# Kernel optimization log

Measured on AMD Instinct MI355X. Metric: run time of the kernel, lower is better.

The kernel has to match this reference:

```python
import jax, jax.numpy as jnp
import numpy as np

B, S, D, H = 4, 1024, 1024, 16  # batch, seq_len, num_hiddens, num_heads
NEG = -1e6  # mask value used by the source's _sequence_mask


def setup_inputs() -> dict:
    key = jax.random.key(0)
    ks = jax.random.split(key, 8)
    f = lambda k, sh: (jax.random.normal(k, sh, dtype=jnp.float32) * 0.02)
    return {
        "queries": f(ks[0], (B, S, D)),
        "keys": f(ks[1], (B, S, D)),
        "values": f(ks[2], (B, S, D)),
        "valid_lens": jax.random.randint(ks[3], (B,), 1, S + 1),
        "Wq": f(ks[4], (D, D)),
        "Wk": f(ks[5], (D, D)),
        "Wv": f(ks[6], (D, D)),
        "Wo": f(ks[7], (D, D)),
    }


def reference(queries, keys, values, valid_lens, Wq, Wk, Wv, Wo):
    dh = D // H

    def split_heads(x):  # [B,S,D] -> [B,H,S,dh]
        return x.reshape(B, S, H, dh).transpose(0, 2, 1, 3)

    q = split_heads(queries @ Wq)
    k = split_heads(keys @ Wk)
    v = split_heads(values @ Wv)

    scores = jnp.einsum("bhqd,bhkd->bhqk", q, k) / jnp.sqrt(jnp.float32(dh))
    # per-batch key mask broadcast over heads and query positions: [B,1,1,S]
    mask = (jnp.arange(S)[None, :] < valid_lens[:, None])[:, None, None, :]
    scores = jnp.where(mask, scores, NEG)        # pre-softmax set to -1e6
    attn = jax.nn.softmax(scores, axis=-1)
    attn = jnp.where(mask, attn, 0.0)            # post-softmax zeroing (source quirk)
    out = jnp.einsum("bhqk,bhkd->bhqd", attn, v)  # [B,H,S,dh]
    # source uses permute(0,2,3,1): head-interleaved concat order
    concat = out.transpose(0, 2, 3, 1).reshape(B, S, D)
    return concat @ Wo
```

## Files before the change

### kernel.cpp

```cpp
#include <hip/hip_runtime.h>
#include <hip/hip_bf16.h>

#define BB 4
#define SS 1024
#define DDIM 1024
#define HH 16
#define MROWS (BB * SS)

typedef __attribute__((ext_vector_type(8))) short bf16x8;
typedef __attribute__((ext_vector_type(4))) float f32x4;

static __device__ __forceinline__ short f2bf(float x) {
    union { __hip_bfloat16 h; short s; } u;
    u.h = __float2bfloat16(x);
    return u.s;
}

#define GL_LDS16(gp, lp)                                                      \
    __builtin_amdgcn_global_load_lds(                                         \
        (const __attribute__((address_space(1))) void*)(gp),                  \
        (__attribute__((address_space(3))) void*)(lp), 16, 0, 0)

#define SWZ8(row, s) (((s) ^ ((row) & 7)) << 3)

static __device__ __forceinline__ void transposeW_body(const float* __restrict__ W,
                                                       short* __restrict__ dst,
                                                       int k0, int n0,
                                                       short (*sT)[72], int t) {
    {
        int r = t >> 2, cq = (t & 3) << 4;
        const float* p = W + (size_t)(k0 + r) * DDIM + n0 + cq;
        float4 a = ((const float4*)p)[0], b = ((const float4*)p)[1];
        float4 c = ((const float4*)p)[2], d = ((const float4*)p)[3];
        short* dp = &sT[r][cq];
        dp[0]  = f2bf(a.x); dp[1]  = f2bf(a.y); dp[2]  = f2bf(a.z); dp[3]  = f2bf(a.w);
        dp[4]  = f2bf(b.x); dp[5]  = f2bf(b.y); dp[6]  = f2bf(b.z); dp[7]  = f2bf(b.w);
        dp[8]  = f2bf(c.x); dp[9]  = f2bf(c.y); dp[10] = f2bf(c.z); dp[11] = f2bf(c.w);
        dp[12] = f2bf(d.x); dp[13] = f2bf(d.y); dp[14] = f2bf(d.z); dp[15] = f2bf(d.w);
    }
    __syncthreads();
    {
        int n = t >> 2, kq = (t & 3) << 4;
        bf16x8 o0, o1;
#pragma unroll
        for (int j = 0; j < 8; ++j) o0[j] = sT[kq + j][n];
#pragma unroll
        for (int j = 0; j < 8; ++j) o1[j] = sT[kq + 8 + j][n];
        short* q = dst + (size_t)(n0 + n) * DDIM + k0 + kq;
        *(bf16x8*)q = o0;
        *(bf16x8*)(q + 8) = o1;
    }
}

__global__ __launch_bounds__(256) void prep(const float* __restrict__ X0,
                                            const float* __restrict__ X1,
                                            const float* __restrict__ X2,
                                            const float* __restrict__ W0,
                                            const float* __restrict__ W1,
                                            const float* __restrict__ W2,
                                            short* __restrict__ dstA,
                                            short* __restrict__ Wt,
                                            const int* __restrict__ vlens) {
    __shared__ short sT[64][72];
    const int bx = blockIdx.x;
    const int t = threadIdx.x;
    if (bx >= 6144) {
        const int w = bx - 6144;
        const int z = w >> 8;
        const int rem = w & 255;
        const float* W = (z == 0) ? W0 : (z == 1) ? W1 : W2;
        transposeW_body(W, Wt + (size_t)z * DDIM * DDIM,
                        (rem >> 4) * 64, (rem & 15) * 64, sT, t);
        return;
    }
    const int z = bx >> 11;
    const int blk = bx & 2047;
    const int row0 = blk << 1;
    if (z >= 1) {
        const int bb = row0 >> 10;
        if ((row0 & 1023) >= vlens[bb]) return;
    }
    const float* X = (z == 0) ? X0 : (z == 1) ? X1 : X2;
    short* D = dstA + (size_t)z * MROWS * DDIM;
    const size_t base = (size_t)blk * 2048 + t * 8;
    const float4 x0 = ((const float4*)(X + base))[0];
    const float4 x1 = ((const float4*)(X + base))[1];
    bf16x8 vv;
    vv[0] = f2bf(x0.x); vv[1] = f2bf(x0.y); vv[2] = f2bf(x0.z); vv[3] = f2bf(x0.w);
    vv[4] = f2bf(x1.x); vv[5] = f2bf(x1.y); vv[6] = f2bf(x1.z); vv[7] = f2bf(x1.w);
    *(bf16x8*)(D + base) = vv;
}

__global__ __launch_bounds__(256) void post(const short* __restrict__ v,
                                            short* __restrict__ vT,
                                            const float* __restrict__ Wo,
                                            short* __restrict__ wt_o,
                                            const int* __restrict__ vlens) {
    __shared__ short sT[64][72];
    const int t = threadIdx.x;
    const int z = blockIdx.z;
    if (z == 4) {
        transposeW_body(Wo, wt_o, blockIdx.y * 64, blockIdx.x * 64, sT, t);
        return;
    }
    const int st = blockIdx.x, h = blockIdx.y, bb = z;
    if (st * 64 >= vlens[bb]) return;
#pragma unroll
    for (int j = 0; j < 2; ++j) {
        int c = t + j * 256;
        int sr = c >> 3, co = (c & 7) << 3;
        *(bf16x8*)(&sT[sr][co]) =
            *(const bf16x8*)(v + (size_t)(bb * SS + st * 64 + sr) * DDIM + h * 64 + co);
    }
    __syncthreads();
    {
        int e = t >> 2, sq = (t & 3) << 4;
        bf16x8 o0, o1;
#pragma unroll
        for (int j = 0; j < 8; ++j) o0[j] = sT[sq + j][e];
#pragma unroll
        for (int j = 0; j < 8; ++j) o1[j] = sT[sq + 8 + j][e];
        short* dst = vT + ((size_t)(bb * HH + h) * 64 + e) * SS + st * 64 + sq;
        *(bf16x8*)dst = o0;
        *(bf16x8*)(dst + 8) = o1;
    }
}

__global__ __launch_bounds__(256) void transposeW3(const float* __restrict__ W0,
                                                   const float* __restrict__ W1,
                                                   const float* __restrict__ W2,
                                                   short* __restrict__ Wt) {
    __shared__ short sT[64][72];
    const int z = blockIdx.z;
    const float* W = (z == 0) ? W0 : (z == 1) ? W1 : W2;
    transposeW_body(W, Wt + (size_t)z * DDIM * DDIM,
                    blockIdx.y * 64, blockIdx.x * 64, sT, threadIdx.x);
}

__global__ __launch_bounds__(256) void transposeV(const short* __restrict__ v,
                                                  short* __restrict__ vT,
                                                  const int* __restrict__ vlens) {
    const int st = blockIdx.x, h = blockIdx.y, bb = blockIdx.z;
    if (st * 64 >= vlens[bb]) return;
    __shared__ short sT[64][72];
    const int t = threadIdx.x;
#pragma unroll
    for (int j = 0; j < 2; ++j) {
        int c = t + j * 256;
        int sr = c >> 3, co = (c & 7) << 3;
        *(bf16x8*)(&sT[sr][co]) =
            *(const bf16x8*)(v + (size_t)(bb * SS + st * 64 + sr) * DDIM + h * 64 + co);
    }
    __syncthreads();
    {
        int e = t >> 2, sq = (t & 3) << 4;
        bf16x8 o0, o1;
#pragma unroll
        for (int j = 0; j < 8; ++j) o0[j] = sT[sq + j][e];
#pragma unroll
        for (int j = 0; j < 8; ++j) o1[j] = sT[sq + 8 + j][e];
        short* dst = vT + ((size_t)(bb * HH + h) * 64 + e) * SS + st * 64 + sq;
        *(bf16x8*)dst = o0;
        *(bf16x8*)(dst + 8) = o1;
    }
}

template<bool A_F32, bool C_F32, int BN, bool SKIP>
__global__ __launch_bounds__(256) void gemm(const void* __restrict__ A0v,
                                            const void* __restrict__ A1v,
                                            const void* __restrict__ A2v,
                                            const short* __restrict__ BtBase,
                                            void* __restrict__ C0v,
                                            void* __restrict__ C1v,
                                            void* __restrict__ C2v,
                                            const int* __restrict__ vlens) {
    constexpr int NJ  = BN / 32;
    constexpr int NBX = DDIM / BN;
    constexpr int NPB = 32 * NBX;
    constexpr int BCH = BN / 32;

    __shared__ short sA[128 * 64];
    __shared__ short sB[BN * 64];

    const int tid = threadIdx.x;
    const int lane = tid & 63, wid = tid >> 6;
    const int wr = wid >> 1, wc = wid & 1;
    const int g = lane >> 4, l15 = lane & 15;

    const int blk = blockIdx.x;
    const int z = blk / NPB;
    const int inner = blk % NPB;
    const int xcd = inner & 7, ii = inner >> 3;
    const int by = xcd * 4 + ii / NBX;
    const int bx = ii % NBX;

    if constexpr (SKIP) {
        if (z >= 1 && ((by & 7) << 7) >= vlens[by >> 3]) return;
    }

    const void* Av = (z == 0) ? A0v : (z == 1) ? A1v : A2v;
    const short* Bt = BtBase + (size_t)z * DDIM * DDIM;
    void* Cv = (z == 0) ? C0v : (z == 1) ? C1v : C2v;
    const float* Af = (const float*)Av;
    const short* Ab = (const short*)Av;
    const int K = DDIM;

    f32x4 acc[4][NJ] = {};
    const int nkt = K >> 6;

    for (int t = 0; t < nkt; ++t) {
        const int kt = t << 6;
        __syncthreads();

        if constexpr (A_F32) {
            float4 ra[4][2];
#pragma unroll
            for (int j = 0; j < 4; ++j) {
                int c = tid + j * 256;
                int row = c >> 3, s = c & 7;
                const float* p = Af + (size_t)(by * 128 + row) * K + kt + s * 8;
                ra[j][0] = ((const float4*)p)[0];
                ra[j][1] = ((const float4*)p)[1];
            }
#pragma unroll
            for (int j = 0; j < 4; ++j) {
                int c = tid + j * 256;
                int row = c >> 3, s = c & 7;
                bf16x8 vv;
                vv[0] = f2bf(ra[j][0].x); vv[1] = f2bf(ra[j][0].y);
                vv[2] = f2bf(ra[j][0].z); vv[3] = f2bf(ra[j][0].w);
                vv[4] = f2bf(ra[j][1].x); vv[5] = f2bf(ra[j][1].y);
                vv[6] = f2bf(ra[j][1].z); vv[7] = f2bf(ra[j][1].w);
                *(bf16x8*)(&sA[row * 64 + SWZ8(row, s)]) = vv;
            }
        } else {
#pragma unroll
            for (int j = 0; j < 4; ++j) {
                int c = tid + j * 256;
                int row = c >> 3, sp = c & 7;
                GL_LDS16(Ab + (size_t)(by * 128 + row) * K + kt + SWZ8(row, sp),
                         (char*)&sA[0] + c * 16);
            }
        }
#pragma unroll
        for (int j = 0; j < BCH; ++j) {
            int c = tid + j * 256;
            int row = c >> 3, sp = c & 7;
            GL_LDS16(Bt + (size_t)(bx * BN + row) * K + kt + SWZ8(row, sp),
                     (char*)&sB[0] + c * 16);
        }
        __syncthreads();

        bf16x8 af[4][2], bfr[NJ][2];
#pragma unroll
        for (int i = 0; i < 4; ++i) {
            int row = wr * 64 + i * 16 + l15;
#pragma unroll
            for (int kh = 0; kh < 2; ++kh) {
                int s = kh * 4 + g;
                af[i][kh] = *(const bf16x8*)(&sA[row * 64 + SWZ8(row, s)]);
            }
        }
#pragma unroll
        for (int j = 0; j < NJ; ++j) {
            int row = wc * (BN / 2) + j * 16 + l15;
#pragma unroll
            for (int kh = 0; kh < 2; ++kh) {
                int s = kh * 4 + g;
                bfr[j][kh] = *(const bf16x8*)(&sB[row * 64 + SWZ8(row, s)]);
            }
        }
#pragma unroll
        for (int kh = 0; kh < 2; ++kh)
#pragma unroll
            for (int i = 0; i < 4; ++i)
#pragma unroll
                for (int j = 0; j < NJ; ++j)
                    acc[i][j] = __builtin_amdgcn_mfma_f32_16x16x32_bf16(af[i][kh], bfr[j][kh], acc[i][j], 0, 0, 0);
    }

#pragma unroll
    for (int i = 0; i < 4; ++i)
#pragma unroll
        for (int j = 0; j < NJ; ++j)
#pragma unroll
            for (int r = 0; r < 4; ++r) {
                int row = by * 128 + wr * 64 + i * 16 + g * 4 + r;
                int col = bx * BN + wc * (BN / 2) + j * 16 + l15;
                if constexpr (C_F32)
                    ((float*)Cv)[(size_t)row * DDIM + col] = acc[i][j][r];
                else
                    ((short*)Cv)[(size_t)row * DDIM + col] = f2bf(acc[i][j][r]);
            }
}

template<bool TRV>
__global__ __launch_bounds__(256) void attn(const short* __restrict__ q,
                                            const short* __restrict__ k,
                                            const short* __restrict__ v,
                                            const int* __restrict__ vlens,
                                            short* __restrict__ att) {
    const int blk = blockIdx.x;
    const int qt = blk >> 6;
    const int hb = blk & 63;
    const int bb = hb & 3;
    const int h  = hb >> 2;

    const int tid = threadIdx.x;
    const int lane = tid & 63, wid = tid >> 6;
    const int g = lane >> 4, l15 = lane & 15;
    const int vlen = vlens[bb];

    __shared__ short sK[2][64 * 64];
    __shared__ short sV[2][64 * 64];
    __shared__ short sP[4][16 * 64];

    const int srow = qt * 64 + wid * 16 + l15;
    const short* qrow = q + ((size_t)(bb * SS + srow)) * DDIM + h * 64;
    bf16x8 qf[2];
    qf[0] = *(const bf16x8*)(qrow + g * 8);
    qf[1] = *(const bf16x8*)(qrow + 32 + g * 8);

    float lsum[4] = {0.f, 0.f, 0.f, 0.f};
    f32x4 oacc[4] = {};

    const int key0 = tid >> 3, key1 = (tid + 256) >> 3, sp = tid & 7;
    const int d0 = (tid & 7) << 3;
    const short* vTb = v + ((size_t)(bb * HH + h) * 64) * SS;

    const int ntiles = (vlen + 63) >> 6;

    {
        GL_LDS16(k + ((size_t)(bb * SS + key0)) * DDIM + h * 64 + ((sp ^ (key0 & 7)) << 3),
                 (char*)&sK[0][0] + tid * 16);
        GL_LDS16(k + ((size_t)(bb * SS + key1)) * DDIM + h * 64 + ((sp ^ (key1 & 7)) << 3),
                 (char*)&sK[0][0] + (tid + 256) * 16);
        if constexpr (TRV) {
            GL_LDS16(vTb + (size_t)key0 * SS + ((sp ^ (key0 & 7)) << 3),
                     (char*)&sV[0][0] + tid * 16);
            GL_LDS16(vTb + (size_t)key1 * SS + ((sp ^ (key1 & 7)) << 3),
                     (char*)&sV[0][0] + (tid + 256) * 16);
        } else {
            bf16x8 v0 = *(const bf16x8*)(v + ((size_t)(bb * SS + key0)) * DDIM + h * 64 + d0);
            bf16x8 v1 = *(const bf16x8*)(v + ((size_t)(bb * SS + key1)) * DDIM + h * 64 + d0);
#pragma unroll
            for (int e = 0; e < 8; ++e) {
                int e0 = d0 + e;
                sV[0][e0 * 64 + (((key0 >> 3) ^ (e0 & 7)) << 3) + (key0 & 7)] = v0[e];
                sV[0][e0 * 64 + (((key1 >> 3) ^ (e0 & 7)) << 3) + (key1 & 7)] = v1[e];
            }
        }
    }
    __syncthreads();

    for (int t = 0; t < ntiles; ++t) {
        const int cur = t & 1, nxt = cur ^ 1;
        const int kb = t * 64;
        const bool pre = (t + 1 < ntiles);

        bf16x8 vr0, vr1;
        if (pre) {
            const int kb2 = kb + 64;
            GL_LDS16(k + ((size_t)(bb * SS + kb2 + key0)) * DDIM + h * 64 + ((sp ^ (key0 & 7)) << 3),
                     (char*)&sK[nxt][0] + tid * 16);
            GL_LDS16(k + ((size_t)(bb * SS + kb2 + key1)) * DDIM + h * 64 + ((sp ^ (key1 & 7)) << 3),
                     (char*)&sK[nxt][0] + (tid + 256) * 16);
            if constexpr (TRV) {
                GL_LDS16(vTb + (size_t)key0 * SS + kb2 + ((sp ^ (key0 & 7)) << 3),
                         (char*)&sV[nxt][0] + tid * 16);
                GL_LDS16(vTb + (size_t)key1 * SS + kb2 + ((sp ^ (key1 & 7)) << 3),
                         (char*)&sV[nxt][0] + (tid + 256) * 16);
            } else {
                vr0 = *(const bf16x8*)(v + ((size_t)(bb * SS + kb2 + key0)) * DDIM + h * 64 + d0);
                vr1 = *(const bf16x8*)(v + ((size_t)(bb * SS + kb2 + key1)) * DDIM + h * 64 + d0);
            }
        }

        f32x4 sacc[4] = {};
#pragma unroll
        for (int kg = 0; kg < 4; ++kg) {
            int row = kg * 16 + l15;
#pragma unroll
            for (int kh = 0; kh < 2; ++kh) {
                int s = kh * 4 + g;
                bf16x8 kf = *(const bf16x8*)(&sK[cur][row * 64 + ((s ^ (row & 7)) << 3)]);
                sacc[kg] = __builtin_amdgcn_mfma_f32_16x16x32_bf16(qf[kh], kf, sacc[kg], 0, 0, 0);
            }
        }

#pragma unroll
        for (int r = 0; r < 4; ++r) {
            float p[4], ls = 0.f;
#pragma unroll
            for (int kg = 0; kg < 4; ++kg) {
                float s = fminf(sacc[kg][r] * 0.125f, 60.0f);
                if (kb + kg * 16 + l15 >= vlen) s = -1e30f;
                p[kg] = __expf(s);
                ls += p[kg];
            }
            lsum[r] += ls;
            const int srw = g * 4 + r;
#pragma unroll
            for (int kg = 0; kg < 4; ++kg) {
                int col = kg * 16 + l15;
                sP[wid][srw * 64 + (((col >> 3) ^ (srw & 7)) << 3) + (col & 7)] = f2bf(p[kg]);
            }
        }

        bf16x8 pf[2];
#pragma unroll
        for (int kh = 0; kh < 2; ++kh) {
            int s = kh * 4 + g;
            pf[kh] = *(const bf16x8*)(&sP[wid][l15 * 64 + ((s ^ (l15 & 7)) << 3)]);
        }
#pragma unroll
        for (int n = 0; n < 4; ++n) {
            const int e = n * 16 + l15;
#pragma unroll
            for (int kh = 0; kh < 2; ++kh) {
                int s = kh * 4 + g;
                bf16x8 vf = *(const bf16x8*)(&sV[cur][e * 64 + ((s ^ (e & 7)) << 3)]);
                oacc[n] = __builtin_amdgcn_mfma_f32_16x16x32_bf16(pf[kh], vf, oacc[n], 0, 0, 0);
            }
        }

        if constexpr (!TRV) {
            if (pre) {
#pragma unroll
                for (int e = 0; e < 8; ++e) {
                    int e0 = d0 + e;
                    sV[nxt][e0 * 64 + (((key0 >> 3) ^ (e0 & 7)) << 3) + (key0 & 7)] = vr0[e];
                    sV[nxt][e0 * 64 + (((key1 >> 3) ^ (e0 & 7)) << 3) + (key1 & 7)] = vr1[e];
                }
            }
        }
        __syncthreads();
    }

#pragma unroll
    for (int r = 0; r < 4; ++r) {
        float rs = lsum[r];
#pragma unroll
        for (int off = 1; off < 16; off <<= 1)
            rs += __shfl_xor(rs, off);
        lsum[r] = rs;
    }

#pragma unroll
    for (int n = 0; n < 4; ++n)
#pragma unroll
        for (int r = 0; r < 4; ++r) {
            float o = oacc[n][r] / lsum[r];
            int sg = qt * 64 + wid * 16 + g * 4 + r;
            int e = n * 16 + l15;
            att[((size_t)(bb * SS + sg)) * DDIM + e * HH + h] = f2bf(o);
        }
}

extern "C" void kernel_launch(void* const* d_in, const int* in_sizes, int n_in,
                              void* d_out, int out_size, void* d_ws, size_t ws_size,
                              hipStream_t stream) {
    const float* queries = (const float*)d_in[0];
    const float* keys    = (const float*)d_in[1];
    const float* values  = (const float*)d_in[2];
    const int*   vlens   = (const int*)d_in[3];
    const float* Wq      = (const float*)d_in[4];
    const float* Wk      = (const float*)d_in[5];
    const float* Wv      = (const float*)d_in[6];
    const float* Wo      = (const float*)d_in[7];
    float* out = (float*)d_out;

    short* ws = (short*)d_ws;
    const size_t sz = (size_t)MROWS * DDIM;
    short* q_ws   = ws;
    short* k_ws   = ws + sz;
    short* v_ws   = ws + 2 * sz;
    short* att_ws = ws + 3 * sz;
    short* wt3  = att_ws;

    const size_t regionB = sz * sizeof(short);
    const bool big = ws_size >= 7 * regionB;
    const bool mid = ws_size >= 5 * regionB;

    if (big) {
        short* qb = ws + 4 * sz;
        short* kb = ws + 5 * sz;
        short* vb = ws + 6 * sz;
        prep<<<dim3(6912), 256, 0, stream>>>(queries, keys, values,
                                             Wq, Wk, Wv, qb, wt3, vlens);
        gemm<false, false, 128, true><<<dim3(768), 256, 0, stream>>>(
            qb, kb, vb, wt3, q_ws, k_ws, v_ws, vlens);
        post<<<dim3(16, 16, 5), 256, 0, stream>>>(v_ws, qb, Wo, vb, vlens);
        attn<true><<<dim3(1024), 256, 0, stream>>>(q_ws, k_ws, qb, vlens, att_ws);
        gemm<false, true, 64, false><<<dim3(512), 256, 0, stream>>>(
            att_ws, att_ws, att_ws, vb, out, out, out, vlens);
    } else if (mid) {
        short* vT = ws + 4 * sz;
        short* wt_o = q_ws;
        transposeW3<<<dim3(16, 16, 3), 256, 0, stream>>>(Wq, Wk, Wv, wt3);
        gemm<true, false, 128, true><<<dim3(768), 256, 0, stream>>>(
            queries, keys, values, wt3, q_ws, k_ws, v_ws, vlens);
        transposeV<<<dim3(16, 16, 4), 256, 0, stream>>>(v_ws, vT, vlens);
        attn<true><<<dim3(1024), 256, 0, stream>>>(q_ws, k_ws, vT, vlens, att_ws);
        transposeW3<<<dim3(16, 16, 1), 256, 0, stream>>>(Wo, Wo, Wo, wt_o);
        gemm<false, true, 64, false><<<dim3(512), 256, 0, stream>>>(
            att_ws, att_ws, att_ws, wt_o, out, out, out, vlens);
    } else {
        short* wt_o = q_ws;
        transposeW3<<<dim3(16, 16, 3), 256, 0, stream>>>(Wq, Wk, Wv, wt3);
        gemm<true, false, 128, true><<<dim3(768), 256, 0, stream>>>(
            queries, keys, values, wt3, q_ws, k_ws, v_ws, vlens);
        attn<false><<<dim3(1024), 256, 0, stream>>>(q_ws, k_ws, v_ws, vlens, att_ws);
        transposeW3<<<dim3(16, 16, 1), 256, 0, stream>>>(Wo, Wo, Wo, wt_o);
        gemm<false, true, 64, false><<<dim3(512), 256, 0, stream>>>(
            att_ws, att_ws, att_ws, wt_o, out, out, out, vlens);
    }
}
```

Before: 94.66 us.

## Fuse V transpose into QKV GEMM epilogue and Wo transpose into attention

The QKV projection GEMM now writes V directly in head-transposed layout by staging its tile through shared memory in the epilogue, and the Wo weight transpose runs as extra blocks prepended to the attention launch. Together these remove the separate post kernel and its launch, plus a full round-trip of V through global memory. In exchange the GEMM epilogue for V gains an extra LDS pass and barrier, and the attention kernel uses one merged shared buffer and a larger grid.

```diff
diff --git a/kernel.cpp b/kernel.cpp
--- a/kernel.cpp
+++ b/kernel.cpp
@@ -91,41 +91,6 @@
     *(bf16x8*)(D + base) = vv;
 }
 
-__global__ __launch_bounds__(256) void post(const short* __restrict__ v,
-                                            short* __restrict__ vT,
-                                            const float* __restrict__ Wo,
-                                            short* __restrict__ wt_o,
-                                            const int* __restrict__ vlens) {
-    __shared__ short sT[64][72];
-    const int t = threadIdx.x;
-    const int z = blockIdx.z;
-    if (z == 4) {
-        transposeW_body(Wo, wt_o, blockIdx.y * 64, blockIdx.x * 64, sT, t);
-        return;
-    }
-    const int st = blockIdx.x, h = blockIdx.y, bb = z;
-    if (st * 64 >= vlens[bb]) return;
-#pragma unroll
-    for (int j = 0; j < 2; ++j) {
-        int c = t + j * 256;
-        int sr = c >> 3, co = (c & 7) << 3;
-        *(bf16x8*)(&sT[sr][co]) =
-            *(const bf16x8*)(v + (size_t)(bb * SS + st * 64 + sr) * DDIM + h * 64 + co);
-    }
-    __syncthreads();
-    {
-        int e = t >> 2, sq = (t & 3) << 4;
-        bf16x8 o0, o1;
-#pragma unroll
-        for (int j = 0; j < 8; ++j) o0[j] = sT[sq + j][e];
-#pragma unroll
-        for (int j = 0; j < 8; ++j) o1[j] = sT[sq + 8 + j][e];
-        short* dst = vT + ((size_t)(bb * HH + h) * 64 + e) * SS + st * 64 + sq;
-        *(bf16x8*)dst = o0;
-        *(bf16x8*)(dst + 8) = o1;
-    }
-}
-
 __global__ __launch_bounds__(256) void transposeW3(const float* __restrict__ W0,
                                                    const float* __restrict__ W1,
                                                    const float* __restrict__ W2,
@@ -165,7 +130,7 @@
     }
 }
 
-template<bool A_F32, bool C_F32, int BN, bool SKIP>
+template<bool A_F32, bool C_F32, int BN, bool SKIP, bool TRC>
 __global__ __launch_bounds__(256) void gemm(const void* __restrict__ A0v,
                                             const void* __restrict__ A1v,
                                             const void* __restrict__ A2v,
@@ -179,8 +144,9 @@
     constexpr int NPB = 32 * NBX;
     constexpr int BCH = BN / 32;
 
-    __shared__ short sA[128 * 64];
-    __shared__ short sB[BN * 64];
+    __shared__ short smem[128 * 64 + BN * 64];
+    short* sA = smem;
+    short* sB = smem + 128 * 64;
 
     const int tid = threadIdx.x;
     const int lane = tid & 63, wid = tid >> 6;
@@ -239,7 +205,7 @@
                 int c = tid + j * 256;
                 int row = c >> 3, sp = c & 7;
                 GL_LDS16(Ab + (size_t)(by * 128 + row) * K + kt + SWZ8(row, sp),
-                         (char*)&sA[0] + c * 16);
+                         (char*)sA + c * 16);
             }
         }
 #pragma unroll
@@ -247,7 +213,7 @@
             int c = tid + j * 256;
             int row = c >> 3, sp = c & 7;
             GL_LDS16(Bt + (size_t)(bx * BN + row) * K + kt + SWZ8(row, sp),
-                     (char*)&sB[0] + c * 16);
+                     (char*)sB + c * 16);
         }
         __syncthreads();
 
@@ -277,6 +243,39 @@
 #pragma unroll
                 for (int j = 0; j < NJ; ++j)
                     acc[i][j] = __builtin_amdgcn_mfma_f32_16x16x32_bf16(af[i][kh], bfr[j][kh], acc[i][j], 0, 0, 0);
+    }
+
+    if constexpr (TRC && BN == 128) {
+        if (z == 2) {
+            __syncthreads();
+            short* sT = smem;
+#pragma unroll
+            for (int i = 0; i < 4; ++i)
+#pragma unroll
+                for (int j = 0; j < NJ; ++j)
+#pragma unroll
+                    for (int r = 0; r < 4; ++r) {
+                        int row = wr * 64 + i * 16 + g * 4 + r;
+                        int col = wc * 64 + j * 16 + l15;
+                        sT[col * 128 + ((((row >> 3) ^ (col & 7)) << 3) | (row & 7))] =
+                            f2bf(acc[i][j][r]);
+                    }
+            __syncthreads();
+            {
+                int col = tid >> 1, half = tid & 1;
+                int cg = bx * 128 + col;
+                int h = cg >> 6, e = cg & 63;
+                size_t R = ((size_t)(by >> 3) * HH + h) * 64 + e;
+                short* dst = (short*)Cv + R * SS + (size_t)(by & 7) * 128 + half * 64;
+#pragma unroll
+                for (int m = 0; m < 8; ++m) {
+                    int mm = half * 8 + m;
+                    bf16x8 ch = *(const bf16x8*)(&sT[col * 128 + ((mm ^ (col & 7)) << 3)]);
+                    *(bf16x8*)(dst + m * 8) = ch;
+                }
+            }
+            return;
+        }
     }
 
 #pragma unroll
@@ -294,26 +293,35 @@
             }
 }
 
-template<bool TRV>
+template<bool TRV, bool WOT>
 __global__ __launch_bounds__(256) void attn(const short* __restrict__ q,
                                             const short* __restrict__ k,
                                             const short* __restrict__ v,
                                             const int* __restrict__ vlens,
-                                            short* __restrict__ att) {
-    const int blk = blockIdx.x;
+                                            short* __restrict__ att,
+                                            const float* __restrict__ Wo,
+                                            short* __restrict__ wt_o) {
+    __shared__ short asmem[20480];
+    const int tid = threadIdx.x;
+    int blk = blockIdx.x;
+    if constexpr (WOT) {
+        if (blk < 256) {
+            transposeW_body(Wo, wt_o, (blk >> 4) * 64, (blk & 15) * 64,
+                            (short (*)[72])asmem, tid);
+            return;
+        }
+        blk -= 256;
+    }
+
     const int qt = blk >> 6;
     const int hb = blk & 63;
     const int bb = hb & 3;
     const int h  = hb >> 2;
 
-    const int tid = threadIdx.x;
     const int lane = tid & 63, wid = tid >> 6;
     const int g = lane >> 4, l15 = lane & 15;
     const int vlen = vlens[bb];
-
-    __shared__ short sK[2][64 * 64];
-    __shared__ short sV[2][64 * 64];
-    __shared__ short sP[4][16 * 64];
+    const int pOff = 16384 + wid * 1024;
 
     const int srow = qt * 64 + wid * 16 + l15;
     const short* qrow = q + ((size_t)(bb * SS + srow)) * DDIM + h * 64;
@@ -332,22 +340,22 @@
 
     {
         GL_LDS16(k + ((size_t)(bb * SS + key0)) * DDIM + h * 64 + ((sp ^ (key0 & 7)) << 3),
-                 (char*)&sK[0][0] + tid * 16);
+                 (char*)&asmem[0] + tid * 16);
         GL_LDS16(k + ((size_t)(bb * SS + key1)) * DDIM + h * 64 + ((sp ^ (key1 & 7)) << 3),
-                 (char*)&sK[0][0] + (tid + 256) * 16);
+                 (char*)&asmem[0] + (tid + 256) * 16);
         if constexpr (TRV) {
             GL_LDS16(vTb + (size_t)key0 * SS + ((sp ^ (key0 & 7)) << 3),
-                     (char*)&sV[0][0] + tid * 16);
+                     (char*)&asmem[8192] + tid * 16);
             GL_LDS16(vTb + (size_t)key1 * SS + ((sp ^ (key1 & 7)) << 3),
-                     (char*)&sV[0][0] + (tid + 256) * 16);
+                     (char*)&asmem[8192] + (tid + 256) * 16);
         } else {
             bf16x8 v0 = *(const bf16x8*)(v + ((size_t)(bb * SS + key0)) * DDIM + h * 64 + d0);
             bf16x8 v1 = *(const bf16x8*)(v + ((size_t)(bb * SS + key1)) * DDIM + h * 64 + d0);
 #pragma unroll
             for (int e = 0; e < 8; ++e) {
                 int e0 = d0 + e;
-                sV[0][e0 * 64 + (((key0 >> 3) ^ (e0 & 7)) << 3) + (key0 & 7)] = v0[e];
-                sV[0][e0 * 64 + (((key1 >> 3) ^ (e0 & 7)) << 3) + (key1 & 7)] = v1[e];
+                asmem[8192 + e0 * 64 + (((key0 >> 3) ^ (e0 & 7)) << 3) + (key0 & 7)] = v0[e];
+                asmem[8192 + e0 * 64 + (((key1 >> 3) ^ (e0 & 7)) << 3) + (key1 & 7)] = v1[e];
             }
         }
     }
@@ -355,6 +363,8 @@
 
     for (int t = 0; t < ntiles; ++t) {
         const int cur = t & 1, nxt = cur ^ 1;
+        const int kOffC = cur * 4096, kOffN = nxt * 4096;
+        const int vOffC = 8192 + cur * 4096, vOffN = 8192 + nxt * 4096;
         const int kb = t * 64;
         const bool pre = (t + 1 < ntiles);
 
@@ -362,14 +372,14 @@
         if (pre) {
             const int kb2 = kb + 64;
             GL_LDS16(k + ((size_t)(bb * SS + kb2 + key0)) * DDIM + h * 64 + ((sp ^ (key0 & 7)) << 3),
-                     (char*)&sK[nxt][0] + tid * 16);
+                     (char*)&asmem[0] + kOffN * 2 + tid * 16);
             GL_LDS16(k + ((size_t)(bb * SS + kb2 + key1)) * DDIM + h * 64 + ((sp ^ (key1 & 7)) << 3),
-                     (char*)&sK[nxt][0] + (tid + 256) * 16);
+                     (char*)&asmem[0] + kOffN * 2 + (tid + 256) * 16);
             if constexpr (TRV) {
                 GL_LDS16(vTb + (size_t)key0 * SS + kb2 + ((sp ^ (key0 & 7)) << 3),
-                         (char*)&sV[nxt][0] + tid * 16);
+                         (char*)&asmem[0] + vOffN * 2 + tid * 16);
                 GL_LDS16(vTb + (size_t)key1 * SS + kb2 + ((sp ^ (key1 & 7)) << 3),
-                         (char*)&sV[nxt][0] + (tid + 256) * 16);
+                         (char*)&asmem[0] + vOffN * 2 + (tid + 256) * 16);
             } else {
                 vr0 = *(const bf16x8*)(v + ((size_t)(bb * SS + kb2 + key0)) * DDIM + h * 64 + d0);
                 vr1 = *(const bf16x8*)(v + ((size_t)(bb * SS + kb2 + key1)) * DDIM + h * 64 + d0);
@@ -383,7 +393,7 @@
 #pragma unroll
             for (int kh = 0; kh < 2; ++kh) {
                 int s = kh * 4 + g;
-                bf16x8 kf = *(const bf16x8*)(&sK[cur][row * 64 + ((s ^ (row & 7)) << 3)]);
+                bf16x8 kf = *(const bf16x8*)(&asmem[kOffC + row * 64 + ((s ^ (row & 7)) << 3)]);
                 sacc[kg] = __builtin_amdgcn_mfma_f32_16x16x32_bf16(qf[kh], kf, sacc[kg], 0, 0, 0);
             }
         }
@@ -403,7 +413,7 @@
 #pragma unroll
             for (int kg = 0; kg < 4; ++kg) {
                 int col = kg * 16 + l15;
-                sP[wid][srw * 64 + (((col >> 3) ^ (srw & 7)) << 3) + (col & 7)] = f2bf(p[kg]);
+                asmem[pOff + srw * 64 + (((col >> 3) ^ (srw & 7)) << 3) + (col & 7)] = f2bf(p[kg]);
             }
         }
 
@@ -411,7 +421,7 @@
 #pragma unroll
         for (int kh = 0; kh < 2; ++kh) {
             int s = kh * 4 + g;
-            pf[kh] = *(const bf16x8*)(&sP[wid][l15 * 64 + ((s ^ (l15 & 7)) << 3)]);
+            pf[kh] = *(const bf16x8*)(&asmem[pOff + l15 * 64 + ((s ^ (l15 & 7)) << 3)]);
         }
 #pragma unroll
         for (int n = 0; n < 4; ++n) {
@@ -419,7 +429,7 @@
 #pragma unroll
             for (int kh = 0; kh < 2; ++kh) {
                 int s = kh * 4 + g;
-                bf16x8 vf = *(const bf16x8*)(&sV[cur][e * 64 + ((s ^ (e & 7)) << 3)]);
+                bf16x8 vf = *(const bf16x8*)(&asmem[vOffC + e * 64 + ((s ^ (e & 7)) << 3)]);
                 oacc[n] = __builtin_amdgcn_mfma_f32_16x16x32_bf16(pf[kh], vf, oacc[n], 0, 0, 0);
             }
         }
@@ -429,8 +439,8 @@
 #pragma unroll
                 for (int e = 0; e < 8; ++e) {
                     int e0 = d0 + e;
-                    sV[nxt][e0 * 64 + (((key0 >> 3) ^ (e0 & 7)) << 3) + (key0 & 7)] = vr0[e];
-                    sV[nxt][e0 * 64 + (((key1 >> 3) ^ (e0 & 7)) << 3) + (key1 & 7)] = vr1[e];
+                    asmem[vOffN + e0 * 64 + (((key0 >> 3) ^ (e0 & 7)) << 3) + (key0 & 7)] = vr0[e];
+                    asmem[vOffN + e0 * 64 + (((key1 >> 3) ^ (e0 & 7)) << 3) + (key1 & 7)] = vr1[e];
                 }
             }
         }
@@ -474,9 +484,9 @@
     const size_t sz = (size_t)MROWS * DDIM;
     short* q_ws   = ws;
     short* k_ws   = ws + sz;
-    short* v_ws   = ws + 2 * sz;
+    short* reg2   = ws + 2 * sz;
     short* att_ws = ws + 3 * sz;
-    short* wt3  = att_ws;
+    short* wt3    = att_ws;
 
     const size_t regionB = sz * sizeof(short);
     const bool big = ws_size >= 7 * regionB;
@@ -488,31 +498,33 @@
         short* vb = ws + 6 * sz;
         prep<<<dim3(6912), 256, 0, stream>>>(queries, keys, values,
                                              Wq, Wk, Wv, qb, wt3, vlens);
-        gemm<false, false, 128, true><<<dim3(768), 256, 0, stream>>>(
-            qb, kb, vb, wt3, q_ws, k_ws, v_ws, vlens);
-        post<<<dim3(16, 16, 5), 256, 0, stream>>>(v_ws, qb, Wo, vb, vlens);
-        attn<true><<<dim3(1024), 256, 0, stream>>>(q_ws, k_ws, qb, vlens, att_ws);
-        gemm<false, true, 64, false><<<dim3(512), 256, 0, stream>>>(
+        gemm<false, false, 128, true, true><<<dim3(768), 256, 0, stream>>>(
+            qb, kb, vb, wt3, q_ws, k_ws, reg2, vlens);
+        attn<true, true><<<dim3(1280), 256, 0, stream>>>(
+            q_ws, k_ws, reg2, vlens, att_ws, Wo, vb);
+        gemm<false, true, 64, false, false><<<dim3(512), 256, 0, stream>>>(
             att_ws, att_ws, att_ws, vb, out, out, out, vlens);
     } else if (mid) {
         short* vT = ws + 4 * sz;
         short* wt_o = q_ws;
         transposeW3<<<dim3(16, 16, 3), 256, 0, stream>>>(Wq, Wk, Wv, wt3);
-        gemm<true, false, 128, true><<<dim3(768), 256, 0, stream>>>(
-            queries, keys, values, wt3, q_ws, k_ws, v_ws, vlens);
-        transposeV<<<dim3(16, 16, 4), 256, 0, stream>>>(v_ws, vT, vlens);
-        attn<true><<<dim3(1024), 256, 0, stream>>>(q_ws, k_ws, vT, vlens, att_ws);
+        gemm<true, false, 128, true, false><<<dim3(768), 256, 0, stream>>>(
+            queries, keys, values, wt3, q_ws, k_ws, reg2, vlens);
+        transposeV<<<dim3(16, 16, 4), 256, 0, stream>>>(reg2, vT, vlens);
+        attn<true, false><<<dim3(1024), 256, 0, stream>>>(
+            q_ws, k_ws, vT, vlens, att_ws, Wo, wt_o);
         transposeW3<<<dim3(16, 16, 1), 256, 0, stream>>>(Wo, Wo, Wo, wt_o);
-        gemm<false, true, 64, false><<<dim3(512), 256, 0, stream>>>(
+        gemm<false, true, 64, false, false><<<dim3(512), 256, 0, stream>>>(
             att_ws, att_ws, att_ws, wt_o, out, out, out, vlens);
     } else {
         short* wt_o = q_ws;
         transposeW3<<<dim3(16, 16, 3), 256, 0, stream>>>(Wq, Wk, Wv, wt3);
-        gemm<true, false, 128, true><<<dim3(768), 256, 0, stream>>>(
-            queries, keys, values, wt3, q_ws, k_ws, v_ws, vlens);
-        attn<false><<<dim3(1024), 256, 0, stream>>>(q_ws, k_ws, v_ws, vlens, att_ws);
+        gemm<true, false, 128, true, false><<<dim3(768), 256, 0, stream>>>(
+            queries, keys, values, wt3, q_ws, k_ws, reg2, vlens);
+        attn<false, false><<<dim3(1024), 256, 0, stream>>>(
+            q_ws, k_ws, reg2, vlens, att_ws, Wo, wt_o);
         transposeW3<<<dim3(16, 16, 1), 256, 0, stream>>>(Wo, Wo, Wo, wt_o);
-        gemm<false, true, 64, false><<<dim3(512), 256, 0, stream>>>(
+        gemm<false, true, 64, false, false><<<dim3(512), 256, 0, stream>>>(
             att_ws, att_ws, att_ws, wt_o, out, out, out, vlens);
     }
 }
```

Measured after the change: 90.90 us. -4.0%, faster.
